# Kernel optimization log

Hardware: AMD Instinct MI355X
Metric: run time of the kernel (lower is better)

Reference implementation:

```python
import jax, jax.numpy as jnp
import numpy as np

B, S, F = 4096, 128, 8
H1, H2 = 64, 32


def setup_inputs() -> dict:
    key = jax.random.key(0)
    ks = jax.random.split(key, 12)
    rn = lambda k, shape, scale: jax.random.normal(k, shape, dtype=jnp.float32) * scale
    return {
        "x": rn(ks[0], (B, S, F), 1.0),
        "time": jax.random.uniform(ks[1], (B, 1), dtype=jnp.float32),
        # linear_combine: (S*F + 1) -> S*F
        "W_combine": rn(ks[2], (S * F, S * F + 1), 1.0 / np.sqrt(S * F + 1)),
        "b_combine": jnp.zeros((S * F,), jnp.float32),
        # LSTM layer 1 (bias=False), gate order i,f,g,o like torch
        "W_ih1": rn(ks[3], (4 * H1, F), 1.0 / np.sqrt(H1)),
        "W_hh1": rn(ks[4], (4 * H1, H1), 1.0 / np.sqrt(H1)),
        # LSTM layer 2 (bias=True)
        "W_ih2": rn(ks[5], (4 * H2, H1), 1.0 / np.sqrt(H2)),
        "W_hh2": rn(ks[6], (4 * H2, H2), 1.0 / np.sqrt(H2)),
        "b_ih2": rn(ks[7], (4 * H2,), 0.05),
        "b_hh2": rn(ks[8], (4 * H2,), 0.05),
        # l_linear_supervised: (H2*S) -> 1
        "W_out": rn(ks[9], (1, H2 * S), 1.0 / np.sqrt(H2 * S)),
        "b_out": jnp.zeros((1,), jnp.float32),
    }


def _lstm(x, W_ih, W_hh, b):
    """batch_first LSTM, zero initial state. x: [B,S,D] -> hidden seq [B,S,H]."""
    Bq = x.shape[0]
    H = W_hh.shape[1]
    # precompute input contribution for all timesteps: [B,S,4H]
    xg = jnp.einsum('bsd,gd->bsg', x, W_ih) + b

    def step(carry, xg_t):
        h, c = carry
        g = xg_t + h @ W_hh.T
        i, f, gg, o = jnp.split(g, 4, axis=-1)  # torch gate order i,f,g,o
        c = jax.nn.sigmoid(f) * c + jax.nn.sigmoid(i) * jnp.tanh(gg)
        h = jax.nn.sigmoid(o) * jnp.tanh(c)
        return (h, c), h

    h0 = jnp.zeros((Bq, H), x.dtype)
    (_, _), hs = jax.lax.scan(step, (h0, h0), jnp.swapaxes(xg, 0, 1))
    return jnp.swapaxes(hs, 0, 1)


def reference(x, time, W_combine, b_combine, W_ih1, W_hh1, W_ih2, W_hh2,
              b_ih2, b_hh2, W_out, b_out):
    Bq = x.shape[0]
    # future_time_as_input == 1 branch: flatten, append time, linear + relu
    xf = jnp.concatenate([x.reshape(Bq, -1), time.reshape(Bq, -1)], axis=1)
    xf = jax.nn.relu(xf @ W_combine.T + b_combine)
    x1 = xf.reshape(Bq, S, F)
    h1 = _lstm(x1, W_ih1, W_hh1, jnp.zeros((4 * H1,), x.dtype))  # [B,S,64]
    h2 = _lstm(h1, W_ih2, W_hh2, b_ih2 + b_hh2)                   # [B,S,32]
    return h2.reshape(Bq, -1) @ W_out.T + b_out                   # [B,1]
```

## Files before the change

### kernel.cpp

```cpp
#include <hip/hip_runtime.h>
#include <math.h>


typedef _Float16 f16x8 __attribute__((ext_vector_type(8)));
typedef float f32x4 __attribute__((ext_vector_type(4)));

union H8 { uint4 q; _Float16 h[8]; f16x8 v; };

#define MF(A, B, C) __builtin_amdgcn_mfma_f32_16x16x32_f16(A, B, C, 0, 0, 0)
#define LOG2E 1.44269504f

__device__ __forceinline__ float sigm_pre(float y) {
  return __builtin_amdgcn_rcpf(1.f + __builtin_amdgcn_exp2f(-y));
}
__device__ __forceinline__ float tanh_pre2(float y2) {
  return 1.f - 2.f * __builtin_amdgcn_rcpf(1.f + __builtin_amdgcn_exp2f(y2));
}
__device__ __forceinline__ float tanh_raw(float c) {
  return 1.f - 2.f * __builtin_amdgcn_rcpf(1.f + __builtin_amdgcn_exp2f(c * 2.88539008f));
}
__device__ __forceinline__ unsigned pkrtz(float a, float b) {
  return __builtin_bit_cast(unsigned, __builtin_amdgcn_cvt_pkrtz(a, b));
}

__global__ __launch_bounds__(256) void cvt_x(
    const float* __restrict__ x, unsigned* __restrict__ x16)
{
  const int idx = blockIdx.x * 256 + threadIdx.x;
  const float4* src = (const float4*)x;
  float4 a = src[2 * idx], b = src[2 * idx + 1];
  uint4 o = {pkrtz(a.x, a.y), pkrtz(a.z, a.w), pkrtz(b.x, b.y), pkrtz(b.z, b.w)};
  ((uint4*)x16)[idx] = o;
}

#define CROW 72

__global__ __launch_bounds__(256, 2) void combine_mfma(
    const _Float16* __restrict__ xh, const float* __restrict__ tme,
    const float* __restrict__ Wc, const float* __restrict__ bc,
    unsigned* __restrict__ x1u)
{
  __shared__ __align__(16) _Float16 sA[2][128][CROW];
  __shared__ __align__(16) _Float16 sB[2][64][CROW];
  __shared__ float sT[128];
  __shared__ float sWl[64];
  __shared__ float sBc[64];
  _Float16 (*Cst)[CROW] = sA[0];

  const int tid = threadIdx.x;
  const int lane = tid & 63;
  const int w = tid >> 6;
  const int r = lane & 15, grp = lane >> 4;
  const int M0 = blockIdx.y * 128, N0 = blockIdx.x * 64;

  if (tid < 128) sT[tid] = tme[M0 + tid];
  else if (tid < 192) sWl[tid - 128] = Wc[(size_t)(N0 + tid - 128) * 1025 + 1024];
  else sBc[tid - 192] = bc[N0 + tid - 192];

#define STAGE_A(KT, BUF)                                                       \
  _Pragma("unroll") for (int i = 0; i < 4; ++i) {                              \
    int idx = tid + i * 256;                                                   \
    int row = idx >> 3, kq = idx & 7;                                          \
    uint4 v = *(const uint4*)&xh[(size_t)(M0 + row) * 1024 + (KT) + kq * 8];   \
    *(uint4*)&sA[BUF][row][kq * 8] = v;                                        \
  }
#define STAGE_B(KT, BUF)                                                       \
  _Pragma("unroll") for (int i = 0; i < 4; ++i) {                              \
    int idx = tid + i * 256;                                                   \
    int row = idx >> 4, kq = idx & 15;                                         \
    float4 v = *(const float4*)&Wc[(size_t)(N0 + row) * 1025 + (KT) + kq * 4]; \
    *(uint2*)&sB[BUF][row][kq * 4] = uint2{pkrtz(v.x, v.y), pkrtz(v.z, v.w)};  \
  }

  f32x4 acc[2][4];
#pragma unroll
  for (int i = 0; i < 2; ++i)
#pragma unroll
    for (int j = 0; j < 4; ++j) acc[i][j] = f32x4{0.f, 0.f, 0.f, 0.f};

  STAGE_A(0, 0);
  STAGE_B(0, 0);
  __syncthreads();

  int cur = 0;
  for (int kt = 0; kt < 1024; kt += 64) {
    H8 af[2][2], bf[4][2];
#pragma unroll
    for (int i = 0; i < 2; ++i)
#pragma unroll
      for (int c = 0; c < 2; ++c)
        af[i][c].q = *(const uint4*)&sA[cur][w * 32 + i * 16 + r][c * 32 + grp * 8];
#pragma unroll
    for (int j = 0; j < 4; ++j)
#pragma unroll
      for (int c = 0; c < 2; ++c)
        bf[j][c].q = *(const uint4*)&sB[cur][j * 16 + r][c * 32 + grp * 8];

    if (kt < 960) {
      STAGE_A(kt + 64, cur ^ 1);
      STAGE_B(kt + 64, cur ^ 1);
    }

#pragma unroll
    for (int i = 0; i < 2; ++i)
#pragma unroll
      for (int j = 0; j < 4; ++j) {
        acc[i][j] = MF(af[i][0].v, bf[j][0].v, acc[i][j]);
        acc[i][j] = MF(af[i][1].v, bf[j][1].v, acc[i][j]);
      }
    __syncthreads();
    cur ^= 1;
  }
#undef STAGE_A
#undef STAGE_B

#pragma unroll
  for (int i = 0; i < 2; ++i) {
#pragma unroll
    for (int j = 0; j < 4; ++j) {
      int n = j * 16 + r;
      float wl = sWl[n], bv = sBc[n];
#pragma unroll
      for (int q = 0; q < 4; ++q) {
        int mm = w * 32 + i * 16 + 4 * grp + q;
        float v = acc[i][j][q] + sT[mm] * wl + bv;
        Cst[mm][n] = (_Float16)fmaxf(v, 0.f);
      }
    }
  }
  __syncthreads();
#pragma unroll
  for (int i = 0; i < 4; ++i) {
    int idx = tid + i * 256;
    int row = idx >> 3, c8 = idx & 7;
    uint4 v = *(const uint4*)&Cst[row][c8 * 8];
    *(uint4*)&x1u[(size_t)(M0 + row) * 512 + (N0 >> 1) + c8 * 4] = v;
  }
}

#define ROW1 72
#define ROW2 40

__global__ __launch_bounds__(512, 2) void lstm_fused_mfma(
    const unsigned* __restrict__ x1u,
    const float* __restrict__ Wih1, const float* __restrict__ Whh1,
    const float* __restrict__ Wih2, const float* __restrict__ Whh2,
    const float* __restrict__ bih2, const float* __restrict__ bhh2,
    const float* __restrict__ Wout, const float* __restrict__ bout,
    float* __restrict__ out)
{
  __shared__ __align__(16) unsigned sxw[128 * 16 * 4];
  __shared__ float sWoT[32 * 132];
  __shared__ __align__(16) unsigned short sh1[2][16][ROW1];
  __shared__ __align__(16) unsigned short sh2[2][16][ROW2];
  __shared__ float sOut[8][16];

  const int tid = threadIdx.x;
  const int lane = tid & 63;
  const int w = tid >> 6;
  const int vw = w >> 1;
  const int wsub = w & 1;
  const int col = lane & 15;
  const int grp = lane >> 4;
  const int b0 = blockIdx.x * 16;

  const int m1 = col >> 2, g1 = col & 3;
  const float gsc = (g1 == 2) ? 2.f * LOG2E : LOG2E;
  f16x8 A1h[2][2];
  f16x8 A1x[2];
#pragma unroll
  for (int jj = 0; jj < 2; ++jj) {
    const int wr = g1 * 64 + vw * 16 + 4 * m1 + (2 * wsub + jj);
#pragma unroll
    for (int c = 0; c < 2; ++c) {
      H8 f;
#pragma unroll
      for (int q = 0; q < 8; ++q)
        f.h[q] = (_Float16)(Whh1[wr * 64 + c * 32 + grp * 8 + q] * gsc);
      A1h[jj][c] = f.v;
    }
    H8 fx;
#pragma unroll
    for (int q = 0; q < 8; ++q)
      fx.h[q] = (grp == 0) ? (_Float16)(Wih1[wr * 8 + q] * gsc) : (_Float16)0.f;
    A1x[jj] = fx.v;
  }
  f16x8 A2[3];
  const int u = 2 * vw + wsub;
  {
    const int wr = g1 * 32 + 4 * u + m1;
#pragma unroll
    for (int c = 0; c < 3; ++c) {
      H8 f;
#pragma unroll
      for (int q = 0; q < 8; ++q) {
        float wv = (c < 2) ? Wih2[wr * 64 + c * 32 + grp * 8 + q]
                           : Whh2[wr * 32 + grp * 8 + q];
        f.h[q] = (_Float16)(wv * gsc);
      }
      A2[c] = f.v;
    }
  }
  const int h2o = 4 * u + grp;
  f32x4 b2q;
#pragma unroll
  for (int r = 0; r < 4; ++r) {
    const float rs = (r == 2) ? 2.f * LOG2E : LOG2E;
    b2q[r] = (bih2[r * 32 + h2o] + bhh2[r * 32 + h2o]) * rs;
  }
  const f32x4 zq = {0.f, 0.f, 0.f, 0.f};

  for (int idx = tid; idx < 4096; idx += 512) {
    int t = idx >> 5, h = idx & 31;
    sWoT[h * 132 + t] = Wout[idx];
  }
  {
    unsigned short* z = &sh1[0][0][0];
    for (int i2 = tid; i2 < 2 * 16 * ROW1; i2 += 512) z[i2] = 0;
    unsigned short* z2 = &sh2[0][0][0];
    for (int i2 = tid; i2 < 2 * 16 * ROW2; i2 += 512) z2[i2] = 0;
  }
  for (int idx = tid; idx < 16 * 512; idx += 512) {
    int bb = idx >> 9, rem = idx & 511;
    int t = rem >> 2, pr = rem & 3;
    sxw[t * 64 + bb * 4 + pr] = x1u[(size_t)(b0 + bb) * 512 + rem];
  }
  __syncthreads();

  float c1a = 0.f, c1b = 0.f, c2 = 0.f, accO = 0.f;

#define PHASE(T, CUR, DO_L1, DO_L2)                                            \
  {                                                                            \
    H8 s0, s1, s2;                                                             \
    s0.q = *(const uint4*)&sh1[CUR][col][grp * 8];                             \
    s1.q = *(const uint4*)&sh1[CUR][col][32 + grp * 8];                        \
    s2.q = *(const uint4*)&sh2[CUR][col][grp * 8];                             \
    if (DO_L2) {                                                               \
      const float won = sWoT[h2o * 132 + (T) - 1];                             \
      f32x4 a = MF(A2[2], s2.v, b2q);                                          \
      a = MF(A2[0], s0.v, a);                                                  \
      a = MF(A2[1], s1.v, a);                                                  \
      float ig = sigm_pre(a[0]), fg = sigm_pre(a[1]);                          \
      float tg = tanh_pre2(a[2]), og = sigm_pre(a[3]);                         \
      float cc = fg * c2 + ig * tg;                                            \
      c2 = cc;                                                                 \
      float hn = og * tanh_raw(cc);                                            \
      accO = fmaf(hn, won, accO);                                              \
      *(_Float16*)&sh2[(CUR) ^ 1][col][h2o] = (_Float16)hn;                    \
    }                                                                          \
    if (DO_L1) {                                                               \
      H8 sx;                                                                   \
      sx.q = *(const uint4*)&sxw[(T) * 64 + col * 4];                          \
      f32x4 a0 = MF(A1x[0], sx.v, zq);                                         \
      f32x4 a1 = MF(A1x[1], sx.v, zq);                                         \
      a0 = MF(A1h[0][0], s0.v, a0);                                            \
      a1 = MF(A1h[1][0], s0.v, a1);                                            \
      a0 = MF(A1h[0][1], s1.v, a0);                                            \
      a1 = MF(A1h[1][1], s1.v, a1);                                            \
      float ig0 = sigm_pre(a0[0]), fg0 = sigm_pre(a0[1]);                      \
      float tg0 = tanh_pre2(a0[2]), og0 = sigm_pre(a0[3]);                     \
      float cc0 = fg0 * c1a + ig0 * tg0;                                       \
      c1a = cc0;                                                               \
      float h0 = og0 * tanh_raw(cc0);                                          \
      float ig1 = sigm_pre(a1[0]), fg1 = sigm_pre(a1[1]);                      \
      float tg1 = tanh_pre2(a1[2]), og1 = sigm_pre(a1[3]);                     \
      float cc1 = fg1 * c1b + ig1 * tg1;                                       \
      c1b = cc1;                                                               \
      float h1v = og1 * tanh_raw(cc1);                                         \
      *(unsigned*)&sh1[(CUR) ^ 1][col][vw * 16 + 4 * grp + 2 * wsub] =         \
          pkrtz(h0, h1v);                                                      \
    }                                                                          \
    __syncthreads();                                                           \
  }

  PHASE(0, 0, true, false);
  PHASE(1, 1, true, true);
  for (int tt = 1; tt < 64; ++tt) {
    const int t0 = 2 * tt;
    PHASE(t0, 0, true, true);
    PHASE(t0 + 1, 1, true, true);
  }
  PHASE(128, 0, false, true);
#undef PHASE

  accO += __shfl_xor(accO, 16);
  accO += __shfl_xor(accO, 32);
  if (grp == 0) sOut[u][col] = accO;
  __syncthreads();
  if (tid < 16) {
    float s = bout[0];
#pragma unroll
    for (int q = 0; q < 8; ++q) s += sOut[q][tid];
    out[b0 + tid] = s;
  }
}

extern "C" void kernel_launch(void* const* d_in, const int* in_sizes, int n_in,
                              void* d_out, int out_size, void* d_ws, size_t ws_size,
                              hipStream_t stream) {
  const float* x    = (const float*)d_in[0];
  const float* tme  = (const float*)d_in[1];
  const float* Wc   = (const float*)d_in[2];
  const float* bc   = (const float*)d_in[3];
  const float* Wih1 = (const float*)d_in[4];
  const float* Whh1 = (const float*)d_in[5];
  const float* Wih2 = (const float*)d_in[6];
  const float* Whh2 = (const float*)d_in[7];
  const float* bih2 = (const float*)d_in[8];
  const float* bhh2 = (const float*)d_in[9];
  const float* Wout = (const float*)d_in[10];
  const float* bout = (const float*)d_in[11];
  float* outp = (float*)d_out;
  unsigned* x1u = (unsigned*)d_ws;
  unsigned* x16 = x1u + (size_t)4096 * 512;

  cvt_x<<<2048, 256, 0, stream>>>(x, x16);
  dim3 gA(16, 32);
  combine_mfma<<<gA, 256, 0, stream>>>((const _Float16*)x16, tme, Wc, bc, x1u);
  lstm_fused_mfma<<<256, 512, 0, stream>>>(x1u, Wih1, Whh1, Wih2, Whh2,
                                           bih2, bhh2, Wout, bout, outp);
}
```

Measured before the change: 106.0 us.

## Widen combine GEMM tile to 128x128 and merge LSTM gate math into one reciprocal

The combine GEMM now uses 512-thread blocks, each computing a 128x128 output tile in dynamic shared memory, where before 256-thread blocks each computed 128x64. This halves the grid and the number of times the A operand is re-read. Separately, the LSTM cell update folds the input, forget and candidate gate sigmoids/tanh into one algebraic expression that needs a single reciprocal. That cuts transcendental work on the serial recurrence but can lose accuracy or overflow for large gate pre-activations, and the larger GEMM tile lowers occupancy.

```diff
diff --git a/kernel.cpp b/kernel.cpp
--- a/kernel.cpp
+++ b/kernel.cpp
@@ -13,11 +13,17 @@
 __device__ __forceinline__ float sigm_pre(float y) {
   return __builtin_amdgcn_rcpf(1.f + __builtin_amdgcn_exp2f(-y));
 }
-__device__ __forceinline__ float tanh_pre2(float y2) {
-  return 1.f - 2.f * __builtin_amdgcn_rcpf(1.f + __builtin_amdgcn_exp2f(y2));
-}
 __device__ __forceinline__ float tanh_raw(float c) {
   return 1.f - 2.f * __builtin_amdgcn_rcpf(1.f + __builtin_amdgcn_exp2f(c * 2.88539008f));
+}
+__device__ __forceinline__ float lstm_c(float yi, float yf, float yg2, float cold) {
+  float Ei = __builtin_amdgcn_exp2f(-yi);
+  float Ef = __builtin_amdgcn_exp2f(-yf);
+  float Eg = __builtin_amdgcn_exp2f(yg2);
+  float Pf = 1.f + Ef;
+  float t1 = (1.f + Ei) * (1.f + Eg);
+  float num = fmaf(Eg - 1.f, Pf, cold * t1);
+  return num * __builtin_amdgcn_rcpf(Pf * t1);
 }
 __device__ __forceinline__ unsigned pkrtz(float a, float b) {
   return __builtin_bit_cast(unsigned, __builtin_amdgcn_cvt_pkrtz(a, b));
@@ -35,38 +41,40 @@
 
 #define CROW 72
 
-__global__ __launch_bounds__(256, 2) void combine_mfma(
+__global__ __launch_bounds__(512, 1) void combine_mfma(
     const _Float16* __restrict__ xh, const float* __restrict__ tme,
     const float* __restrict__ Wc, const float* __restrict__ bc,
     unsigned* __restrict__ x1u)
 {
-  __shared__ __align__(16) _Float16 sA[2][128][CROW];
-  __shared__ __align__(16) _Float16 sB[2][64][CROW];
-  __shared__ float sT[128];
-  __shared__ float sWl[64];
-  __shared__ float sBc[64];
-  _Float16 (*Cst)[CROW] = sA[0];
+  extern __shared__ __align__(16) char smraw[];
+  _Float16 (*sA)[128][CROW] = (_Float16 (*)[128][CROW])(smraw);
+  _Float16 (*sB)[128][CROW] = (_Float16 (*)[128][CROW])(smraw + 36864);
+  float* sT  = (float*)(smraw + 73728);
+  float* sWl = (float*)(smraw + 74240);
+  float* sBc = (float*)(smraw + 74752);
+  _Float16 (*Cst)[136] = (_Float16 (*)[136])smraw;
 
   const int tid = threadIdx.x;
   const int lane = tid & 63;
   const int w = tid >> 6;
+  const int wm = w & 3, wn = w >> 2;
   const int r = lane & 15, grp = lane >> 4;
-  const int M0 = blockIdx.y * 128, N0 = blockIdx.x * 64;
+  const int M0 = blockIdx.y * 128, N0 = blockIdx.x * 128;
 
   if (tid < 128) sT[tid] = tme[M0 + tid];
-  else if (tid < 192) sWl[tid - 128] = Wc[(size_t)(N0 + tid - 128) * 1025 + 1024];
-  else sBc[tid - 192] = bc[N0 + tid - 192];
+  else if (tid < 256) sWl[tid - 128] = Wc[(size_t)(N0 + tid - 128) * 1025 + 1024];
+  else if (tid < 384) sBc[tid - 256] = bc[N0 + tid - 256];
 
 #define STAGE_A(KT, BUF)                                                       \
-  _Pragma("unroll") for (int i = 0; i < 4; ++i) {                              \
-    int idx = tid + i * 256;                                                   \
-    int row = idx >> 3, kq = idx & 7;                                          \
-    uint4 v = *(const uint4*)&xh[(size_t)(M0 + row) * 1024 + (KT) + kq * 8];   \
-    *(uint4*)&sA[BUF][row][kq * 8] = v;                                        \
+  _Pragma("unroll") for (int i = 0; i < 2; ++i) {                              \
+    int idx = tid + i * 512;                                                   \
+    int row = idx >> 3, c8 = idx & 7;                                          \
+    uint4 v = *(const uint4*)&xh[(size_t)(M0 + row) * 1024 + (KT) + c8 * 8];   \
+    *(uint4*)&sA[BUF][row][c8 * 8] = v;                                        \
   }
 #define STAGE_B(KT, BUF)                                                       \
   _Pragma("unroll") for (int i = 0; i < 4; ++i) {                              \
-    int idx = tid + i * 256;                                                   \
+    int idx = tid + i * 512;                                                   \
     int row = idx >> 4, kq = idx & 15;                                         \
     float4 v = *(const float4*)&Wc[(size_t)(N0 + row) * 1025 + (KT) + kq * 4]; \
     *(uint2*)&sB[BUF][row][kq * 4] = uint2{pkrtz(v.x, v.y), pkrtz(v.z, v.w)};  \
@@ -89,12 +97,12 @@
     for (int i = 0; i < 2; ++i)
 #pragma unroll
       for (int c = 0; c < 2; ++c)
-        af[i][c].q = *(const uint4*)&sA[cur][w * 32 + i * 16 + r][c * 32 + grp * 8];
+        af[i][c].q = *(const uint4*)&sA[cur][wm * 32 + i * 16 + r][c * 32 + grp * 8];
 #pragma unroll
     for (int j = 0; j < 4; ++j)
 #pragma unroll
       for (int c = 0; c < 2; ++c)
-        bf[j][c].q = *(const uint4*)&sB[cur][j * 16 + r][c * 32 + grp * 8];
+        bf[j][c].q = *(const uint4*)&sB[cur][wn * 64 + j * 16 + r][c * 32 + grp * 8];
 
     if (kt < 960) {
       STAGE_A(kt + 64, cur ^ 1);
@@ -118,11 +126,11 @@
   for (int i = 0; i < 2; ++i) {
 #pragma unroll
     for (int j = 0; j < 4; ++j) {
-      int n = j * 16 + r;
+      int n = wn * 64 + j * 16 + r;
       float wl = sWl[n], bv = sBc[n];
 #pragma unroll
       for (int q = 0; q < 4; ++q) {
-        int mm = w * 32 + i * 16 + 4 * grp + q;
+        int mm = wm * 32 + i * 16 + 4 * grp + q;
         float v = acc[i][j][q] + sT[mm] * wl + bv;
         Cst[mm][n] = (_Float16)fmaxf(v, 0.f);
       }
@@ -131,10 +139,10 @@
   __syncthreads();
 #pragma unroll
   for (int i = 0; i < 4; ++i) {
-    int idx = tid + i * 256;
-    int row = idx >> 3, c8 = idx & 7;
-    uint4 v = *(const uint4*)&Cst[row][c8 * 8];
-    *(uint4*)&x1u[(size_t)(M0 + row) * 512 + (N0 >> 1) + c8 * 4] = v;
+    int idx = tid + i * 512;
+    int row = idx >> 4, c4 = idx & 15;
+    uint4 v = *(const uint4*)&Cst[row][c4 * 8];
+    *(uint4*)&x1u[(size_t)(M0 + row) * 512 + (N0 >> 1) + c4 * 4] = v;
   }
 }
 
@@ -240,11 +248,9 @@
       f32x4 a = MF(A2[2], s2.v, b2q);                                          \
       a = MF(A2[0], s0.v, a);                                                  \
       a = MF(A2[1], s1.v, a);                                                  \
-      float ig = sigm_pre(a[0]), fg = sigm_pre(a[1]);                          \
-      float tg = tanh_pre2(a[2]), og = sigm_pre(a[3]);                         \
-      float cc = fg * c2 + ig * tg;                                            \
+      float cc = lstm_c(a[0], a[1], a[2], c2);                                 \
       c2 = cc;                                                                 \
-      float hn = og * tanh_raw(cc);                                            \
+      float hn = sigm_pre(a[3]) * tanh_raw(cc);                                \
       accO = fmaf(hn, won, accO);                                              \
       *(_Float16*)&sh2[(CUR) ^ 1][col][h2o] = (_Float16)hn;                    \
     }                                                                          \
@@ -257,16 +263,12 @@
       a1 = MF(A1h[1][0], s0.v, a1);                                            \
       a0 = MF(A1h[0][1], s1.v, a0);                                            \
       a1 = MF(A1h[1][1], s1.v, a1);                                            \
-      float ig0 = sigm_pre(a0[0]), fg0 = sigm_pre(a0[1]);                      \
-      float tg0 = tanh_pre2(a0[2]), og0 = sigm_pre(a0[3]);                     \
-      float cc0 = fg0 * c1a + ig0 * tg0;                                       \
+      float cc0 = lstm_c(a0[0], a0[1], a0[2], c1a);                            \
       c1a = cc0;                                                               \
-      float h0 = og0 * tanh_raw(cc0);                                          \
-      float ig1 = sigm_pre(a1[0]), fg1 = sigm_pre(a1[1]);                      \
-      float tg1 = tanh_pre2(a1[2]), og1 = sigm_pre(a1[3]);                     \
-      float cc1 = fg1 * c1b + ig1 * tg1;                                       \
+      float h0 = sigm_pre(a0[3]) * tanh_raw(cc0);                              \
+      float cc1 = lstm_c(a1[0], a1[1], a1[2], c1b);                            \
       c1b = cc1;                                                               \
-      float h1v = og1 * tanh_raw(cc1);                                         \
+      float h1v = sigm_pre(a1[3]) * tanh_raw(cc1);                             \
       *(unsigned*)&sh1[(CUR) ^ 1][col][vw * 16 + 4 * grp + 2 * wsub] =         \
           pkrtz(h0, h1v);                                                      \
     }                                                                          \
@@ -315,8 +317,12 @@
   unsigned* x16 = x1u + (size_t)4096 * 512;
 
   cvt_x<<<2048, 256, 0, stream>>>(x, x16);
-  dim3 gA(16, 32);
-  combine_mfma<<<gA, 256, 0, stream>>>((const _Float16*)x16, tme, Wc, bc, x1u);
+
+  const size_t smemA = 75264;
+  hipFuncSetAttribute(reinterpret_cast<const void*>(combine_mfma),
+                      hipFuncAttributeMaxDynamicSharedMemorySize, (int)smemA);
+  dim3 gA(8, 32);
+  combine_mfma<<<gA, 512, smemA, stream>>>((const _Float16*)x16, tme, Wc, bc, x1u);
   lstm_fused_mfma<<<256, 512, 0, stream>>>(x1u, Wih1, Whh1, Wih2, Whh2,
                                            bih2, bhh2, Wout, bout, outp);
 }
```

After: 124.3 us. 17.2% more time.
